# Kernel optimization log

Measured on AMD Instinct MI355X. Metric: run time of the kernel, lower is better.

## Reference

```python
import jax, jax.numpy as jnp
import numpy as np

N, T, C, O, K, L = 10000, 8, 16, 64, 16, 3


def setup_inputs():
    key = jax.random.key(0)
    ks = jax.random.split(key, 8)
    s = 0.05
    return dict(
        X=jax.random.normal(ks[0], (N, T, C), jnp.float32),
        As=jax.random.randint(ks[1], (L, T, N, K), 0, N, dtype=jnp.int32),
        key_out=jnp.zeros((1,), jnp.float32),
        key_states=jnp.zeros((2, 1), jnp.float32),
        conv_w=jax.random.normal(ks[2], (L, O, C), jnp.float32) * s,
        conv_b=jax.random.normal(ks[3], (L, O), jnp.float32) * s,
        W_ih=jax.random.normal(ks[4], (L, 4 * O, O), jnp.float32) * s,
        W_hh=jax.random.normal(ks[5], (L, 4 * O, O), jnp.float32) * s,
        b_ih=jax.random.normal(ks[6], (L, 4 * O), jnp.float32) * s,
        b_hh=jax.random.normal(ks[7], (L, 4 * O), jnp.float32) * s,
    )


def _lstm(seq, W_ih, W_hh, b_ih, b_hh):
    # seq: [T, N, O]; PyTorch LSTM gate order i, f, g, o; zero initial state.
    H = W_hh.shape[1]
    n = seq.shape[1]

    def step(carry, xt):
        h, c = carry
        gates = xt @ W_ih.T + h @ W_hh.T + (b_ih + b_hh)
        i, f, g, o = jnp.split(gates, 4, axis=-1)
        c = jax.nn.sigmoid(f) * c + jax.nn.sigmoid(i) * jnp.tanh(g)
        h = jax.nn.sigmoid(o) * jnp.tanh(c)
        return (h, c), h

    init = (jnp.zeros((n, H), seq.dtype), jnp.zeros((n, H), seq.dtype))
    (h, c), ys = jax.lax.scan(step, init, seq)
    return ys, h, c


def _level(x, A, conv_w, conv_b, W_ih, W_hh, b_ih, b_hh):
    # x: [N,T,C], A: [T,N,K] neighbor indices (align=1: ego-subtract)
    xt = jnp.transpose(x, (1, 0, 2))                       # [T,N,C]
    gathered = jax.vmap(lambda xtt, At: xtt[At])(xt, A)    # [T,N,K,C]
    rel = gathered - xt[:, :, None, :]                     # [T,N,K,C]
    # 1x1 conv over channel dim + bias
    feat = jnp.einsum('tnkc,oc->tnko', rel, conv_w) + conv_b  # [T,N,K,O]
    feat = feat.max(axis=2)                                # max-pool over K -> [T,N,O]
    ys, h, c = _lstm(feat, W_ih, W_hh, b_ih, b_hh)         # ys [T,N,O]
    return ys, h, c


def reference(X, As, key_out, key_states, conv_w, conv_b, W_ih, W_hh, b_ih, b_hh):
    # key_out/key_states only used by attention aggregator (type 5); unused here.
    ys, h, c = jax.vmap(_level, in_axes=(None, 0, 0, 0, 0, 0, 0, 0))(
        X, As, conv_w, conv_b, W_ih, W_hh, b_ih, b_hh)     # ys [L,T,N,O], h/c [L,N,O]
    # level_aggregate_type=1: AdaptiveMaxPool2d over the level axis = max over L
    X_out = jnp.transpose(ys.max(axis=0), (1, 0, 2))       # [N,T,O]
    state_h = h.max(axis=0)[:, None, :]                    # [N,1,O]
    state_c = c.max(axis=0)[:, None, :]                    # [N,1,O]
    return X_out, state_h, state_c
```

## Files before the change

### kernel.cpp

```cpp
#include <hip/hip_runtime.h>
#include <hip/hip_bf16.h>

#define NN 10000
#define TT 8
#define LL 3
#define NGRP 625

#define OUT_ELEMS 6400000
#define H_OFF 5120000
#define C_OFF 5760000

typedef __bf16 bf16;
typedef __attribute__((ext_vector_type(8))) __bf16 bf16x8;
typedef __attribute__((ext_vector_type(4))) float f32x4;
typedef __attribute__((ext_vector_type(16))) float f32x16;

__device__ __forceinline__ float sigf(float x) {
    return __builtin_amdgcn_rcpf(1.0f + __expf(-x));
}
__device__ __forceinline__ float tanhf_(float x) {
    return fmaf(2.0f, __builtin_amdgcn_rcpf(1.0f + __expf(-2.0f * x)), -1.0f);
}

__global__ void prep_kernel(const float* __restrict__ W_ih, const float* __restrict__ W_hh,
                            const float* __restrict__ b_ih, const float* __restrict__ b_hh,
                            bf16* __restrict__ wts, float* __restrict__ bias) {
    int id = blockIdx.x * 256 + threadIdx.x;
    if (id < LL * 2 * 256 * 64) {
        int col = id & 63;
        int row = (id >> 6) & 255;
        int mat = (id >> 14) & 1;
        int l = id >> 15;
        const float* src = mat ? W_hh : W_ih;
        float w = src[(l * 256 + row) * 64 + col];
        int kh = col >> 5, nt = row >> 4, nn = row & 15, kk = col & 31;
        wts[((((l * 2 + mat) * 2 + kh) * 16 + nt) * 16 + nn) * 32 + kk] = (bf16)w;
    } else {
        int id2 = id - LL * 2 * 256 * 64;
        if (id2 < LL * 256) bias[id2] = b_ih[id2] + b_hh[id2];
    }
}

__global__ __launch_bounds__(256, 4) void fused_split2_kernel(
    const float* __restrict__ X, const int* __restrict__ As,
    const float* __restrict__ conv_w, const float* __restrict__ conv_b,
    const bf16* __restrict__ wts, const float* __restrict__ bias,
    float* __restrict__ slabs) {
    __shared__ __align__(16) bf16 featL[TT][16][72];
    __shared__ __align__(16) bf16 hlds[2][16][72];
    __shared__ __align__(16) float ylds[2][16][64];

    const int tid = threadIdx.x;
    const int l = blockIdx.x % 3;
    const int grp = blockIdx.x / 3;
    const int node0 = grp * 16;

    const int lane = tid & 63;
    const int wv = tid >> 6;
    const int c16 = lane & 15;
    const int q = lane >> 4;
    const int m = lane & 31;
    const int hh = lane >> 5;
    const int ch0 = hh * 8;
    const int nsub = m >> 4;
    const int kn = m & 15;

    bf16x8 B0, B1;
    {
        const float* w0 = conv_w + ((l * 64 + m) * 16 + ch0);
        f32x4 a = *(const f32x4*)w0, b = *(const f32x4*)(w0 + 4);
        const float* w1 = conv_w + ((l * 64 + 32 + m) * 16 + ch0);
        f32x4 c = *(const f32x4*)w1, d = *(const f32x4*)(w1 + 4);
#pragma unroll
        for (int j = 0; j < 4; ++j) {
            B0[j] = (bf16)a[j]; B0[4 + j] = (bf16)b[j];
            B1[j] = (bf16)c[j]; B1[4 + j] = (bf16)d[j];
        }
    }
    const float cb0 = conv_b[l * 64 + m];
    const float cb1 = conv_b[l * 64 + 32 + m];

#pragma unroll 1
    for (int c = 0; c < 4; ++c) {
        const int pc = 2 * wv + (c & 1);
        const int t0 = (c >> 1) * 4;
        const int gn = node0 + 2 * pc + nsub;

        int aidx[4];
#pragma unroll
        for (int j = 0; j < 4; ++j)
            aidx[j] = As[((long)(l * 8 + t0 + j) * NN + gn) * 16 + kn];
        f32x4 sv[4][2], gv[4][2];
#pragma unroll
        for (int j = 0; j < 4; ++j) {
            const float* sp = X + ((gn * 8 + t0 + j) * 16 + ch0);
            sv[j][0] = *(const f32x4*)sp;
            sv[j][1] = *(const f32x4*)(sp + 4);
        }
#pragma unroll
        for (int j = 0; j < 4; ++j) {
            const float* gp = X + (((long)aidx[j] * 8 + t0 + j) * 16 + ch0);
            gv[j][0] = *(const f32x4*)gp;
            gv[j][1] = *(const f32x4*)(gp + 4);
        }

#pragma unroll
        for (int j = 0; j < 4; ++j) {
            bf16x8 af;
#pragma unroll
            for (int k = 0; k < 4; ++k) {
                af[k]     = (bf16)(gv[j][0][k] - sv[j][0][k]);
                af[4 + k] = (bf16)(gv[j][1][k] - sv[j][1][k]);
            }
            f32x16 D0, D1;
#pragma unroll
            for (int k = 0; k < 16; ++k) { D0[k] = 0.0f; D1[k] = 0.0f; }
            D0 = __builtin_amdgcn_mfma_f32_32x32x16_bf16(af, B0, D0, 0, 0, 0);
            D1 = __builtin_amdgcn_mfma_f32_32x32x16_bf16(af, B1, D1, 0, 0, 0);

            float v00 = D0[0], v01 = D1[0], v10 = D0[8], v11 = D1[8];
#pragma unroll
            for (int k = 1; k < 8; ++k) {
                v00 = fmaxf(v00, D0[k]);     v01 = fmaxf(v01, D1[k]);
                v10 = fmaxf(v10, D0[8 + k]); v11 = fmaxf(v11, D1[8 + k]);
            }
            v00 = fmaxf(v00, __shfl_xor(v00, 32));
            v01 = fmaxf(v01, __shfl_xor(v01, 32));
            v10 = fmaxf(v10, __shfl_xor(v10, 32));
            v11 = fmaxf(v11, __shfl_xor(v11, 32));

            const float sA = hh ? v10 : v00;
            const float sB = hh ? v11 : v01;
            featL[t0 + j][2 * pc + hh][m]      = (bf16)(sA + cb0);
            featL[t0 + j][2 * pc + hh][32 + m] = (bf16)(sB + cb1);
        }
    }

    const bf16* wb = wts + l * 32768;
    const int fo = c16 * 32 + q * 8;
    bf16x8 Bx0[4], Bx1[4], Bh0[4], Bh1[4];
    float brg[4];
#pragma unroll
    for (int g = 0; g < 4; ++g) {
        const int nt = 4 * g + wv;
        Bx0[g] = *(const bf16x8*)(wb + (0 * 16 + nt) * 512 + fo);
        Bx1[g] = *(const bf16x8*)(wb + (1 * 16 + nt) * 512 + fo);
        Bh0[g] = *(const bf16x8*)(wb + (2 * 16 + nt) * 512 + fo);
        Bh1[g] = *(const bf16x8*)(wb + (3 * 16 + nt) * 512 + fo);
        brg[g] = bias[l * 256 + nt * 16 + c16];
    }
    float c_r[4];
#pragma unroll
    for (int r = 0; r < 4; ++r) c_r[r] = 0.0f;

    const int sn = tid >> 4;
    const int sc = (tid & 15) * 4;
    float* slab = slabs + (long)l * OUT_ELEMS;

#pragma unroll
    for (int t = 0; t < TT; ++t) {
        __syncthreads();

        if (t > 0) {
            f32x4 yv = *(const f32x4*)&ylds[(t - 1) & 1][sn][sc];
            *(f32x4*)&slab[((long)(node0 + sn) * 8 + (t - 1)) * 64 + sc] = yv;
        }

        bf16x8 ax0 = *(const bf16x8*)&featL[t][c16][q * 8];
        bf16x8 ax1 = *(const bf16x8*)&featL[t][c16][32 + q * 8];
        bf16x8 ah0, ah1;
        if (t > 0) {
            ah0 = *(const bf16x8*)&hlds[(t + 1) & 1][c16][q * 8];
            ah1 = *(const bf16x8*)&hlds[(t + 1) & 1][c16][32 + q * 8];
        }

        f32x4 acc[4];
#pragma unroll
        for (int g = 0; g < 4; ++g) {
            float b = brg[g];
            acc[g] = (f32x4){b, b, b, b};
            acc[g] = __builtin_amdgcn_mfma_f32_16x16x32_bf16(ax0, Bx0[g], acc[g], 0, 0, 0);
            acc[g] = __builtin_amdgcn_mfma_f32_16x16x32_bf16(ax1, Bx1[g], acc[g], 0, 0, 0);
            if (t > 0) {
                acc[g] = __builtin_amdgcn_mfma_f32_16x16x32_bf16(ah0, Bh0[g], acc[g], 0, 0, 0);
                acc[g] = __builtin_amdgcn_mfma_f32_16x16x32_bf16(ah1, Bh1[g], acc[g], 0, 0, 0);
            }
        }

#pragma unroll
        for (int r = 0; r < 4; ++r) {
            float iv = acc[0][r], fv = acc[1][r], gg = acc[2][r], ov = acc[3][r];
            float c = sigf(fv) * c_r[r] + sigf(iv) * tanhf_(gg);
            c_r[r] = c;
            float h = sigf(ov) * tanhf_(c);
            hlds[t & 1][q * 4 + r][wv * 16 + c16] = (bf16)h;
            ylds[t & 1][q * 4 + r][wv * 16 + c16] = h;
        }
    }

    __syncthreads();
    {
        f32x4 yv = *(const f32x4*)&ylds[1][sn][sc];
        *(f32x4*)&slab[((long)(node0 + sn) * 8 + 7) * 64 + sc] = yv;
        *(f32x4*)&slab[H_OFF + (long)(node0 + sn) * 64 + sc] = yv;
    }
#pragma unroll
    for (int r = 0; r < 4; ++r)
        ylds[0][q * 4 + r][wv * 16 + c16] = c_r[r];
    __syncthreads();
    {
        f32x4 cv = *(const f32x4*)&ylds[0][sn][sc];
        *(f32x4*)&slab[C_OFF + (long)(node0 + sn) * 64 + sc] = cv;
    }
}

__global__ __launch_bounds__(256) void reduce_kernel(
    const float* __restrict__ slabs, float* __restrict__ out) {
    const long i = (long)blockIdx.x * 256 + threadIdx.x;
    const f32x4* s0 = (const f32x4*)slabs;
    const f32x4* s1 = (const f32x4*)(slabs + OUT_ELEMS);
    const f32x4* s2 = (const f32x4*)(slabs + 2L * OUT_ELEMS);
    f32x4 a = s0[i], b = s1[i], c = s2[i], d;
#pragma unroll
    for (int k = 0; k < 4; ++k) d[k] = fmaxf(fmaxf(a[k], b[k]), c[k]);
    ((f32x4*)out)[i] = d;
}

__device__ __forceinline__ void level_body(
    int l, int node0, int tid,
    const float* __restrict__ X, const int* __restrict__ As,
    const float* __restrict__ conv_w, const float* __restrict__ conv_b,
    const bf16* __restrict__ wts, const float* __restrict__ bias,
    bf16 (*featL)[16][72], bf16 (*hlds)[16][72],
    float ymax[TT][4], float hfin[4], float cfin[4], bool accum) {
    const int lane = tid & 63;
    const int wv = tid >> 6;
    const int c16 = lane & 15;
    const int q = lane >> 4;
    const int m = lane & 31;
    const int hh = lane >> 5;
    const int ch0 = hh * 8;
    const int nsub = m >> 4;
    const int kn = m & 15;

    bf16x8 B0, B1;
    {
        const float* w0 = conv_w + ((l * 64 + m) * 16 + ch0);
        f32x4 a = *(const f32x4*)w0, b = *(const f32x4*)(w0 + 4);
        const float* w1 = conv_w + ((l * 64 + 32 + m) * 16 + ch0);
        f32x4 c = *(const f32x4*)w1, d = *(const f32x4*)(w1 + 4);
#pragma unroll
        for (int j = 0; j < 4; ++j) {
            B0[j] = (bf16)a[j]; B0[4 + j] = (bf16)b[j];
            B1[j] = (bf16)c[j]; B1[4 + j] = (bf16)d[j];
        }
    }
    const float cb0 = conv_b[l * 64 + m];
    const float cb1 = conv_b[l * 64 + 32 + m];

#pragma unroll 1
    for (int c = 0; c < 4; ++c) {
        const int pc = 2 * wv + (c & 1);
        const int t0 = (c >> 1) * 4;
        const int gn = node0 + 2 * pc + nsub;

        int aidx[4];
#pragma unroll
        for (int j = 0; j < 4; ++j)
            aidx[j] = As[((long)(l * 8 + t0 + j) * NN + gn) * 16 + kn];
        f32x4 sv[4][2], gv[4][2];
#pragma unroll
        for (int j = 0; j < 4; ++j) {
            const float* sp = X + ((gn * 8 + t0 + j) * 16 + ch0);
            sv[j][0] = *(const f32x4*)sp;
            sv[j][1] = *(const f32x4*)(sp + 4);
        }
#pragma unroll
        for (int j = 0; j < 4; ++j) {
            const float* gp = X + (((long)aidx[j] * 8 + t0 + j) * 16 + ch0);
            gv[j][0] = *(const f32x4*)gp;
            gv[j][1] = *(const f32x4*)(gp + 4);
        }

#pragma unroll
        for (int j = 0; j < 4; ++j) {
            bf16x8 af;
#pragma unroll
            for (int k = 0; k < 4; ++k) {
                af[k]     = (bf16)(gv[j][0][k] - sv[j][0][k]);
                af[4 + k] = (bf16)(gv[j][1][k] - sv[j][1][k]);
            }
            f32x16 D0, D1;
#pragma unroll
            for (int k = 0; k < 16; ++k) { D0[k] = 0.0f; D1[k] = 0.0f; }
            D0 = __builtin_amdgcn_mfma_f32_32x32x16_bf16(af, B0, D0, 0, 0, 0);
            D1 = __builtin_amdgcn_mfma_f32_32x32x16_bf16(af, B1, D1, 0, 0, 0);

            float v00 = D0[0], v01 = D1[0], v10 = D0[8], v11 = D1[8];
#pragma unroll
            for (int k = 1; k < 8; ++k) {
                v00 = fmaxf(v00, D0[k]);     v01 = fmaxf(v01, D1[k]);
                v10 = fmaxf(v10, D0[8 + k]); v11 = fmaxf(v11, D1[8 + k]);
            }
            v00 = fmaxf(v00, __shfl_xor(v00, 32));
            v01 = fmaxf(v01, __shfl_xor(v01, 32));
            v10 = fmaxf(v10, __shfl_xor(v10, 32));
            v11 = fmaxf(v11, __shfl_xor(v11, 32));

            const float sA = hh ? v10 : v00;
            const float sB = hh ? v11 : v01;
            featL[t0 + j][2 * pc + hh][m]      = (bf16)(sA + cb0);
            featL[t0 + j][2 * pc + hh][32 + m] = (bf16)(sB + cb1);
        }
    }

    const bf16* wb = wts + l * 32768;
    const int fo = c16 * 32 + q * 8;
    bf16x8 Bx0[4], Bx1[4], Bh0[4], Bh1[4];
    float brg[4];
#pragma unroll
    for (int g = 0; g < 4; ++g) {
        const int nt = 4 * g + wv;
        Bx0[g] = *(const bf16x8*)(wb + (0 * 16 + nt) * 512 + fo);
        Bx1[g] = *(const bf16x8*)(wb + (1 * 16 + nt) * 512 + fo);
        Bh0[g] = *(const bf16x8*)(wb + (2 * 16 + nt) * 512 + fo);
        Bh1[g] = *(const bf16x8*)(wb + (3 * 16 + nt) * 512 + fo);
        brg[g] = bias[l * 256 + nt * 16 + c16];
    }
    float c_r[4];
#pragma unroll
    for (int r = 0; r < 4; ++r) c_r[r] = 0.0f;

#pragma unroll
    for (int t = 0; t < TT; ++t) {
        __syncthreads();

        bf16x8 ax0 = *(const bf16x8*)&featL[t][c16][q * 8];
        bf16x8 ax1 = *(const bf16x8*)&featL[t][c16][32 + q * 8];
        bf16x8 ah0, ah1;
        if (t > 0) {
            ah0 = *(const bf16x8*)&hlds[(t + 1) & 1][c16][q * 8];
            ah1 = *(const bf16x8*)&hlds[(t + 1) & 1][c16][32 + q * 8];
        }

        f32x4 acc[4];
#pragma unroll
        for (int g = 0; g < 4; ++g) {
            float b = brg[g];
            acc[g] = (f32x4){b, b, b, b};
            acc[g] = __builtin_amdgcn_mfma_f32_16x16x32_bf16(ax0, Bx0[g], acc[g], 0, 0, 0);
            acc[g] = __builtin_amdgcn_mfma_f32_16x16x32_bf16(ax1, Bx1[g], acc[g], 0, 0, 0);
            if (t > 0) {
                acc[g] = __builtin_amdgcn_mfma_f32_16x16x32_bf16(ah0, Bh0[g], acc[g], 0, 0, 0);
                acc[g] = __builtin_amdgcn_mfma_f32_16x16x32_bf16(ah1, Bh1[g], acc[g], 0, 0, 0);
            }
        }

#pragma unroll
        for (int r = 0; r < 4; ++r) {
            float iv = acc[0][r], fv = acc[1][r], gg = acc[2][r], ov = acc[3][r];
            float c = sigf(fv) * c_r[r] + sigf(iv) * tanhf_(gg);
            c_r[r] = c;
            float h = sigf(ov) * tanhf_(c);
            hlds[t & 1][q * 4 + r][wv * 16 + c16] = (bf16)h;
            ymax[t][r] = accum ? fmaxf(ymax[t][r], h) : h;
            if (t == TT - 1) {
                hfin[r] = accum ? fmaxf(hfin[r], h) : h;
                cfin[r] = accum ? fmaxf(cfin[r], c) : c;
            }
        }
    }
}

__global__ __launch_bounds__(256, 3) void fused_kernel(
    const float* __restrict__ X, const int* __restrict__ As,
    const float* __restrict__ conv_w, const float* __restrict__ conv_b,
    const bf16* __restrict__ wts, const float* __restrict__ bias,
    float* __restrict__ out) {
    __shared__ __align__(16) bf16 featL[TT][16][72];
    __shared__ __align__(16) bf16 hlds[2][16][72];

    const int tid = threadIdx.x;
    const int node0 = blockIdx.x * 16;

    float ymax[TT][4], hfin[4], cfin[4];
    for (int l = 0; l < LL; ++l) {
        __syncthreads();
        level_body(l, node0, tid, X, As, conv_w, conv_b, wts, bias,
                   featL, hlds, ymax, hfin, cfin, (l > 0));
    }

    const int lane = tid & 63;
    const int wv = tid >> 6;
    const int c16 = lane & 15;
    const int q = lane >> 4;
    const int col = wv * 16 + c16;
#pragma unroll
    for (int t = 0; t < TT; ++t)
#pragma unroll
        for (int r = 0; r < 4; ++r)
            out[((long)(node0 + q * 4 + r) * 8 + t) * 64 + col] = ymax[t][r];
    float* sh = out + (long)H_OFF;
    float* sc = out + (long)C_OFF;
#pragma unroll
    for (int r = 0; r < 4; ++r) {
        sh[(long)(node0 + q * 4 + r) * 64 + col] = hfin[r];
        sc[(long)(node0 + q * 4 + r) * 64 + col] = cfin[r];
    }
}

extern "C" void kernel_launch(void* const* d_in, const int* in_sizes, int n_in,
                              void* d_out, int out_size, void* d_ws, size_t ws_size,
                              hipStream_t stream) {
    const float* X = (const float*)d_in[0];
    const int* As = (const int*)d_in[1];
    const float* conv_w = (const float*)d_in[4];
    const float* conv_b = (const float*)d_in[5];
    const float* W_ih = (const float*)d_in[6];
    const float* W_hh = (const float*)d_in[7];
    const float* b_ih = (const float*)d_in[8];
    const float* b_hh = (const float*)d_in[9];
    float* out = (float*)d_out;

    char* ws = (char*)d_ws;
    const size_t slabs_bytes = (size_t)3 * OUT_ELEMS * 4;
    const bool big_ws = ws_size >= slabs_bytes + 196608 + 4096;

    if (big_ws) {
        float* slabs = (float*)ws;
        bf16* wts = (bf16*)(ws + slabs_bytes);
        float* bias = (float*)(ws + slabs_bytes + 196608);
        hipLaunchKernelGGL(prep_kernel, dim3(387), dim3(256), 0, stream,
                           W_ih, W_hh, b_ih, b_hh, wts, bias);
        hipLaunchKernelGGL(fused_split2_kernel, dim3(3 * NGRP), dim3(256), 0, stream,
                           X, As, conv_w, conv_b, wts, bias, slabs);
        hipLaunchKernelGGL(reduce_kernel, dim3(OUT_ELEMS / 4 / 256), dim3(256), 0, stream,
                           slabs, out);
    } else {
        bf16* wts = (bf16*)ws;
        float* bias = (float*)(ws + 196608);
        hipLaunchKernelGGL(prep_kernel, dim3(387), dim3(256), 0, stream,
                           W_ih, W_hh, b_ih, b_hh, wts, bias);
        hipLaunchKernelGGL(fused_kernel, dim3(NGRP), dim3(256), 0, stream,
                           X, As, conv_w, conv_b, wts, bias, out);
    }
}
```

Before: 159.5 us.

## Pre-convert X to bf16, factor ego-term out of conv, prefetch gathers

X is converted to bf16 once in the prep kernel, which halves the bytes of the random neighbor gathers. Because the conv is linear, the ego subtraction is taken out of the gather loop: W·x_self is computed once per node and time with one MFMA and subtracted after the max-pool. Neighbor gathers are double-buffered across chunks so loads overlap the MFMA work. The LDS staging of LSTM outputs is removed in favour of direct scattered global stores, which cuts syncs but makes the stores less coalesced and adds bf16 rounding of the ego term.

```diff
diff --git a/kernel.cpp b/kernel.cpp
--- a/kernel.cpp
+++ b/kernel.cpp
@@ -22,9 +22,11 @@
     return fmaf(2.0f, __builtin_amdgcn_rcpf(1.0f + __expf(-2.0f * x)), -1.0f);
 }
 
-__global__ void prep_kernel(const float* __restrict__ W_ih, const float* __restrict__ W_hh,
+__global__ void prep_kernel(const float* __restrict__ X,
+                            const float* __restrict__ W_ih, const float* __restrict__ W_hh,
                             const float* __restrict__ b_ih, const float* __restrict__ b_hh,
-                            bf16* __restrict__ wts, float* __restrict__ bias) {
+                            bf16* __restrict__ wts, float* __restrict__ bias,
+                            bf16* __restrict__ Xh) {
     int id = blockIdx.x * 256 + threadIdx.x;
     if (id < LL * 2 * 256 * 64) {
         int col = id & 63;
@@ -35,20 +37,36 @@
         float w = src[(l * 256 + row) * 64 + col];
         int kh = col >> 5, nt = row >> 4, nn = row & 15, kk = col & 31;
         wts[((((l * 2 + mat) * 2 + kh) * 16 + nt) * 16 + nn) * 32 + kk] = (bf16)w;
-    } else {
+    } else if (id < LL * 2 * 256 * 64 + LL * 256) {
         int id2 = id - LL * 2 * 256 * 64;
-        if (id2 < LL * 256) bias[id2] = b_ih[id2] + b_hh[id2];
-    }
-}
-
-__global__ __launch_bounds__(256, 4) void fused_split2_kernel(
-    const float* __restrict__ X, const int* __restrict__ As,
+        bias[id2] = b_ih[id2] + b_hh[id2];
+    } else if (Xh != nullptr) {
+        int id3 = id - (LL * 2 * 256 * 64 + LL * 256);
+        if (id3 < NN * TT) {
+            const float* xr = X + (long)id3 * 16;
+            f32x4 a = *(const f32x4*)xr,       b = *(const f32x4*)(xr + 4);
+            f32x4 c = *(const f32x4*)(xr + 8), d = *(const f32x4*)(xr + 12);
+            bf16x8 lo, hi;
+#pragma unroll
+            for (int j = 0; j < 4; ++j) {
+                lo[j] = (bf16)a[j]; lo[4 + j] = (bf16)b[j];
+                hi[j] = (bf16)c[j]; hi[4 + j] = (bf16)d[j];
+            }
+            bf16* xo = Xh + (long)id3 * 16;
+            *(bf16x8*)xo = lo;
+            *(bf16x8*)(xo + 8) = hi;
+        }
+    }
+}
+
+__global__ __launch_bounds__(256, 4) void fused_split3_kernel(
+    const bf16* __restrict__ Xh, const int* __restrict__ As,
     const float* __restrict__ conv_w, const float* __restrict__ conv_b,
     const bf16* __restrict__ wts, const float* __restrict__ bias,
     float* __restrict__ slabs) {
     __shared__ __align__(16) bf16 featL[TT][16][72];
     __shared__ __align__(16) bf16 hlds[2][16][72];
-    __shared__ __align__(16) float ylds[2][16][64];
+    __shared__ __align__(16) bf16 swl[128][66];
 
     const int tid = threadIdx.x;
     const int l = blockIdx.x % 3;
@@ -80,43 +98,49 @@
     const float cb0 = conv_b[l * 64 + m];
     const float cb1 = conv_b[l * 64 + 32 + m];
 
-#pragma unroll 1
+    int aidx[4][4];
+#pragma unroll
     for (int c = 0; c < 4; ++c) {
+        const int t0 = (c >> 1) * 4;
+        const int gn = node0 + 2 * (2 * wv + (c & 1)) + nsub;
+#pragma unroll
+        for (int j = 0; j < 4; ++j)
+            aidx[c][j] = As[((long)(l * 8 + t0 + j) * NN + gn) * 16 + kn];
+    }
+
+    {
+        bf16x8 ae = *(const bf16x8*)(Xh + ((long)(node0 * 8 + 32 * wv + m)) * 16 + ch0);
+        f32x16 E0, E1;
+#pragma unroll
+        for (int k = 0; k < 16; ++k) { E0[k] = 0.0f; E1[k] = 0.0f; }
+        E0 = __builtin_amdgcn_mfma_f32_32x32x16_bf16(ae, B0, E0, 0, 0, 0);
+        E1 = __builtin_amdgcn_mfma_f32_32x32x16_bf16(ae, B1, E1, 0, 0, 0);
+#pragma unroll
+        for (int g = 0; g < 16; ++g) {
+            const int r = (g & 3) + 8 * (g >> 2) + 4 * hh;
+            swl[32 * wv + r][m]      = (bf16)E0[g];
+            swl[32 * wv + r][32 + m] = (bf16)E1[g];
+        }
+    }
+
+    bf16x8 gA[4], gB[4];
+    auto gload = [&](int c, bf16x8* dst) {
+        const int t0 = (c >> 1) * 4;
+#pragma unroll
+        for (int j = 0; j < 4; ++j)
+            dst[j] = *(const bf16x8*)(Xh + ((long)aidx[c][j] * 8 + t0 + j) * 16 + ch0);
+    };
+    auto proc = [&](int c, const bf16x8* g) {
+        const int t0 = (c >> 1) * 4;
         const int pc = 2 * wv + (c & 1);
-        const int t0 = (c >> 1) * 4;
-        const int gn = node0 + 2 * pc + nsub;
-
-        int aidx[4];
-#pragma unroll
-        for (int j = 0; j < 4; ++j)
-            aidx[j] = As[((long)(l * 8 + t0 + j) * NN + gn) * 16 + kn];
-        f32x4 sv[4][2], gv[4][2];
-#pragma unroll
-        for (int j = 0; j < 4; ++j) {
-            const float* sp = X + ((gn * 8 + t0 + j) * 16 + ch0);
-            sv[j][0] = *(const f32x4*)sp;
-            sv[j][1] = *(const f32x4*)(sp + 4);
-        }
-#pragma unroll
-        for (int j = 0; j < 4; ++j) {
-            const float* gp = X + (((long)aidx[j] * 8 + t0 + j) * 16 + ch0);
-            gv[j][0] = *(const f32x4*)gp;
-            gv[j][1] = *(const f32x4*)(gp + 4);
-        }
-
-#pragma unroll
-        for (int j = 0; j < 4; ++j) {
-            bf16x8 af;
-#pragma unroll
-            for (int k = 0; k < 4; ++k) {
-                af[k]     = (bf16)(gv[j][0][k] - sv[j][0][k]);
-                af[4 + k] = (bf16)(gv[j][1][k] - sv[j][1][k]);
-            }
+        const int rowb = 32 * wv + (2 * (c & 1) + hh) * 8 + t0;
+#pragma unroll
+        for (int j = 0; j < 4; ++j) {
             f32x16 D0, D1;
 #pragma unroll
             for (int k = 0; k < 16; ++k) { D0[k] = 0.0f; D1[k] = 0.0f; }
-            D0 = __builtin_amdgcn_mfma_f32_32x32x16_bf16(af, B0, D0, 0, 0, 0);
-            D1 = __builtin_amdgcn_mfma_f32_32x32x16_bf16(af, B1, D1, 0, 0, 0);
+            D0 = __builtin_amdgcn_mfma_f32_32x32x16_bf16(g[j], B0, D0, 0, 0, 0);
+            D1 = __builtin_amdgcn_mfma_f32_32x32x16_bf16(g[j], B1, D1, 0, 0, 0);
 
             float v00 = D0[0], v01 = D1[0], v10 = D0[8], v11 = D1[8];
 #pragma unroll
@@ -131,10 +155,17 @@
 
             const float sA = hh ? v10 : v00;
             const float sB = hh ? v11 : v01;
-            featL[t0 + j][2 * pc + hh][m]      = (bf16)(sA + cb0);
-            featL[t0 + j][2 * pc + hh][32 + m] = (bf16)(sB + cb1);
-        }
-    }
+            const float swA = (float)swl[rowb + j][m];
+            const float swB = (float)swl[rowb + j][32 + m];
+            featL[t0 + j][2 * pc + hh][m]      = (bf16)(sA + cb0 - swA);
+            featL[t0 + j][2 * pc + hh][32 + m] = (bf16)(sB + cb1 - swB);
+        }
+    };
+    gload(0, gA); gload(1, gB);
+    proc(0, gA);  gload(2, gA);
+    proc(1, gB);  gload(3, gB);
+    proc(2, gA);
+    proc(3, gB);
 
     const bf16* wb = wts + l * 32768;
     const int fo = c16 * 32 + q * 8;
@@ -153,18 +184,12 @@
 #pragma unroll
     for (int r = 0; r < 4; ++r) c_r[r] = 0.0f;
 
-    const int sn = tid >> 4;
-    const int sc = (tid & 15) * 4;
     float* slab = slabs + (long)l * OUT_ELEMS;
+    const int col = wv * 16 + c16;
 
 #pragma unroll
     for (int t = 0; t < TT; ++t) {
         __syncthreads();
-
-        if (t > 0) {
-            f32x4 yv = *(const f32x4*)&ylds[(t - 1) & 1][sn][sc];
-            *(f32x4*)&slab[((long)(node0 + sn) * 8 + (t - 1)) * 64 + sc] = yv;
-        }
 
         bf16x8 ax0 = *(const bf16x8*)&featL[t][c16][q * 8];
         bf16x8 ax1 = *(const bf16x8*)&featL[t][c16][32 + q * 8];
@@ -193,24 +218,13 @@
             float c = sigf(fv) * c_r[r] + sigf(iv) * tanhf_(gg);
             c_r[r] = c;
             float h = sigf(ov) * tanhf_(c);
-            hlds[t & 1][q * 4 + r][wv * 16 + c16] = (bf16)h;
-            ylds[t & 1][q * 4 + r][wv * 16 + c16] = h;
-        }
-    }
-
-    __syncthreads();
-    {
-        f32x4 yv = *(const f32x4*)&ylds[1][sn][sc];
-        *(f32x4*)&slab[((long)(node0 + sn) * 8 + 7) * 64 + sc] = yv;
-        *(f32x4*)&slab[H_OFF + (long)(node0 + sn) * 64 + sc] = yv;
-    }
-#pragma unroll
-    for (int r = 0; r < 4; ++r)
-        ylds[0][q * 4 + r][wv * 16 + c16] = c_r[r];
-    __syncthreads();
-    {
-        f32x4 cv = *(const f32x4*)&ylds[0][sn][sc];
-        *(f32x4*)&slab[C_OFF + (long)(node0 + sn) * 64 + sc] = cv;
+            hlds[t & 1][q * 4 + r][col] = (bf16)h;
+            slab[((long)(node0 + q * 4 + r) * 8 + t) * 64 + col] = h;
+            if (t == TT - 1) {
+                slab[H_OFF + (long)(node0 + q * 4 + r) * 64 + col] = h;
+                slab[C_OFF + (long)(node0 + q * 4 + r) * 64 + col] = c;
+            }
+        }
     }
 }
 
@@ -424,23 +438,26 @@
 
     char* ws = (char*)d_ws;
     const size_t slabs_bytes = (size_t)3 * OUT_ELEMS * 4;
-    const bool big_ws = ws_size >= slabs_bytes + 196608 + 4096;
+    const size_t xh_bytes = (size_t)NN * TT * 16 * 2;
+    const size_t need = slabs_bytes + 196608 + 4096 + xh_bytes;
+    const bool big_ws = ws_size >= need;
 
     if (big_ws) {
         float* slabs = (float*)ws;
         bf16* wts = (bf16*)(ws + slabs_bytes);
         float* bias = (float*)(ws + slabs_bytes + 196608);
-        hipLaunchKernelGGL(prep_kernel, dim3(387), dim3(256), 0, stream,
-                           W_ih, W_hh, b_ih, b_hh, wts, bias);
-        hipLaunchKernelGGL(fused_split2_kernel, dim3(3 * NGRP), dim3(256), 0, stream,
-                           X, As, conv_w, conv_b, wts, bias, slabs);
+        bf16* Xh = (bf16*)(ws + slabs_bytes + 196608 + 4096);
+        hipLaunchKernelGGL(prep_kernel, dim3(700), dim3(256), 0, stream,
+                           X, W_ih, W_hh, b_ih, b_hh, wts, bias, Xh);
+        hipLaunchKernelGGL(fused_split3_kernel, dim3(3 * NGRP), dim3(256), 0, stream,
+                           Xh, As, conv_w, conv_b, wts, bias, slabs);
         hipLaunchKernelGGL(reduce_kernel, dim3(OUT_ELEMS / 4 / 256), dim3(256), 0, stream,
                            slabs, out);
     } else {
         bf16* wts = (bf16*)ws;
         float* bias = (float*)(ws + 196608);
-        hipLaunchKernelGGL(prep_kernel, dim3(387), dim3(256), 0, stream,
-                           W_ih, W_hh, b_ih, b_hh, wts, bias);
+        hipLaunchKernelGGL(prep_kernel, dim3(700), dim3(256), 0, stream,
+                           X, W_ih, W_hh, b_ih, b_hh, wts, bias, (bf16*)nullptr);
         hipLaunchKernelGGL(fused_kernel, dim3(NGRP), dim3(256), 0, stream,
                            X, As, conv_w, conv_b, wts, bias, out);
     }
```

After: 181.8 us. 1.14x slower.
